# Kernel tuning notes

Hardware: AMD Instinct MI355X
Metric: run time of the kernel (lower is better)

## Reference

```python
import jax, jax.numpy as jnp
import numpy as np

EPS = 1e-6

def _ln(x):
    # LayerNorm without affine, biased variance (matches torch default)
    m = jnp.mean(x, axis=-1, keepdims=True)
    v = jnp.var(x, axis=-1, keepdims=True)
    return (x - m) / jnp.sqrt(v + EPS)

def setup_inputs() -> dict:
    key = jax.random.key(0)
    ks = jax.random.split(key, 12)
    B, N, C = 8, 4096, 768
    H = C * 4
    s = 0.02
    return {
        "x":   jax.random.normal(ks[0], (B, N, C), dtype=jnp.float32),
        "Wq":  jax.random.normal(ks[1], (C, C), dtype=jnp.float32) * s,
        "bq":  jnp.zeros((C,), dtype=jnp.float32),
        "Wkv": jax.random.normal(ks[2], (C, 2 * C), dtype=jnp.float32) * s,
        "bkv": jnp.zeros((2 * C,), dtype=jnp.float32),
        "Wo":  jax.random.normal(ks[3], (C, C), dtype=jnp.float32) * s,
        "bo":  jnp.zeros((C,), dtype=jnp.float32),
        "W1":  jax.random.normal(ks[4], (C, H), dtype=jnp.float32) * s,
        "b1":  jnp.zeros((H,), dtype=jnp.float32),
        "W2":  jax.random.normal(ks[5], (H, C), dtype=jnp.float32) * s,
        "b2":  jnp.zeros((C,), dtype=jnp.float32),
    }

def reference(x, Wq, bq, Wkv, bkv, Wo, bo, W1, b1, W2, b2):
    B, N, C = x.shape
    h = 16
    d = C // h
    scale = d ** -0.5

    xn = _ln(x)                          # norm1 over full sequence
    past = xn[:, :-1, :]                 # [B, N-1, C]
    cur = xn[:, -1, :]                   # [B, C]

    q = (cur @ Wq + bq).reshape(B, h, 1, d)                 # [B,h,1,d]
    kv = past @ Wkv + bkv                                   # [B,N-1,2C]
    k, v = jnp.split(kv, 2, axis=-1)
    k = k.reshape(B, N - 1, h, d).transpose(0, 2, 1, 3)     # [B,h,N-1,d]
    v = v.reshape(B, N - 1, h, d).transpose(0, 2, 1, 3)

    sim = jnp.einsum('bhqd,bhkd->bhqk', q, k) * scale       # [B,h,1,N-1]
    attn = jax.nn.softmax(sim, axis=-1)
    out = jnp.einsum('bhqk,bhkd->bhqd', attn, v)            # [B,h,1,d]
    out = out.transpose(0, 2, 1, 3).reshape(B, C)           # [B,C]
    out = out @ Wo + bo

    last = x[:, -1, :] + out                                # attn residual
    mlp = jax.nn.gelu(_ln(last) @ W1 + b1, approximate=True) @ W2 + b2
    last = last + mlp                                       # mlp residual

    return x.at[:, -1, :].set(last)
```

## Files before the change

kernel.cpp:

```cpp
#include <hip/hip_runtime.h>

#define B_ 8
#define N_ 4096
#define C_ 768
#define NP_ 4095
#define H_ 16
#define D_ 48
#define HID_ 3072
#define SCALE 0.14433756729740643f

typedef unsigned short u16;
typedef unsigned int u32;
typedef __attribute__((ext_vector_type(4))) float f32x4;
typedef __attribute__((ext_vector_type(8))) short short8;

__device__ __forceinline__ u32 f2bf_bits(float f){
  union { float f; u32 i; } v; v.f = f;
  return (v.i + 0x7fffu + ((v.i >> 16) & 1u)) >> 16;
}
__device__ __forceinline__ u16 f2bf(float f){ return (u16)f2bf_bits(f); }
__device__ __forceinline__ u32 pack2(float a, float b){
  return f2bf_bits(a) | (f2bf_bits(b) << 16);
}

__global__ __launch_bounds__(256) void k_q(const float* __restrict__ x,
    const float* __restrict__ Wq, const float* __restrict__ bq,
    float* __restrict__ qv)
{
  int b = blockIdx.y, t = threadIdx.x;
  int j0 = blockIdx.x*32;
  __shared__ float xs[C_];
  __shared__ float red[32][9];
  __shared__ float redA[4], redB[4];
  const float* xr = x + ((size_t)b*N_ + NP_)*C_;
  float v0 = xr[t], v1 = xr[t+256], v2 = xr[t+512];
  float s = v0+v1+v2, q = v0*v0+v1*v1+v2*v2;
  #pragma unroll
  for (int off=32; off; off>>=1){ s += __shfl_xor(s,off); q += __shfl_xor(q,off); }
  int w = t>>6, l = t&63;
  if (l==0){ redA[w]=s; redB[w]=q; }
  __syncthreads();
  s = redA[0]+redA[1]+redA[2]+redA[3];
  q = redB[0]+redB[1]+redB[2]+redB[3];
  float mean = s*(1.f/C_), var = q*(1.f/C_) - mean*mean;
  float rstd = rsqrtf(var + 1e-6f);
  xs[t] = (v0-mean)*rstd; xs[t+256] = (v1-mean)*rstd; xs[t+512] = (v2-mean)*rstd;
  __syncthreads();
  int jl = t&31, part = t>>5;
  const float* wp = Wq + (size_t)(part*96)*C_ + j0 + jl;
  const float* xp = xs + part*96;
  float acc = 0.f;
  #pragma unroll 8
  for (int c=0;c<96;c++) acc += xp[c]*wp[(size_t)c*C_];
  red[jl][part] = acc;
  __syncthreads();
  if (part==0){
    float a = bq[j0+jl];
    #pragma unroll
    for (int p=0;p<8;p++) a += red[jl][p];
    qv[(size_t)b*C_ + j0 + jl] = a;
  }
}

__global__ __launch_bounds__(256) void k_qw(const float* __restrict__ qv,
    const float* __restrict__ Wkv, u16* __restrict__ qWb)
{
  int b = blockIdx.y, t = threadIdx.x;
  int c0 = blockIdx.x*16;
  __shared__ float qs[C_];
  for (int u=t; u<C_; u+=256) qs[u] = qv[(size_t)b*C_+u];
  __syncthreads();
  int h = t&15, cl = t>>4;
  int c = c0 + cl;
  const float* wp = Wkv + (size_t)c*(2*C_) + h*D_;
  const float* qh = qs + h*D_;
  float acc = 0.f;
  #pragma unroll
  for (int d=0; d<D_; d++) acc += qh[d]*wp[d];
  qWb[((size_t)b*H_ + h)*C_ + c] = f2bf(acc);
}

__global__ __launch_bounds__(256) void k_pre(const float* __restrict__ x,
    const u16* __restrict__ qWb, float* __restrict__ outp,
    u16* __restrict__ wrsT, float* __restrict__ denom, float* __restrict__ corr)
{
  int b = blockIdx.y;
  int tid = threadIdx.x;
  int w = tid>>6, l = tid&63;
  int kblk = blockIdx.x*16;
  __shared__ u16 xn[16][776];
  __shared__ float2 stl[16];
  __shared__ float part[4][16][17];
  const size_t xb = (size_t)b*N_*C_;

  #pragma unroll
  for (int i=0;i<4;i++){
    int r = w*4 + i;
    int kt = kblk + r;
    const float4* rp = (const float4*)(x + xb + (size_t)kt*C_);
    float4* op = (float4*)(outp + xb + (size_t)kt*C_);
    float4 v0 = rp[l], v1 = rp[l+64], v2 = rp[l+128];
    op[l] = v0; op[l+64] = v1; op[l+128] = v2;
    float s = v0.x+v0.y+v0.z+v0.w + v1.x+v1.y+v1.z+v1.w + v2.x+v2.y+v2.z+v2.w;
    float q = v0.x*v0.x+v0.y*v0.y+v0.z*v0.z+v0.w*v0.w
            + v1.x*v1.x+v1.y*v1.y+v1.z*v1.z+v1.w*v1.w
            + v2.x*v2.x+v2.y*v2.y+v2.z*v2.z+v2.w*v2.w;
    #pragma unroll
    for (int off=32; off; off>>=1){ s += __shfl_xor(s,off); q += __shfl_xor(q,off); }
    float mean = s*(1.f/C_), var = q*(1.f/C_) - mean*mean;
    float rstd = rsqrtf(var + 1e-6f);
    if (l==0) stl[r] = make_float2(mean, rstd);
    u32* xrow = (u32*)&xn[r][0];
    xrow[2*l]       = pack2((v0.x-mean)*rstd, (v0.y-mean)*rstd);
    xrow[2*l+1]     = pack2((v0.z-mean)*rstd, (v0.w-mean)*rstd);
    xrow[128+2*l]   = pack2((v1.x-mean)*rstd, (v1.y-mean)*rstd);
    xrow[128+2*l+1] = pack2((v1.z-mean)*rstd, (v1.w-mean)*rstd);
    xrow[256+2*l]   = pack2((v2.x-mean)*rstd, (v2.y-mean)*rstd);
    xrow[256+2*l+1] = pack2((v2.z-mean)*rstd, (v2.w-mean)*rstd);
  }
  __syncthreads();

  {
    int arow = l&15;
    int ko = w*192 + (l>>4)*8;
    const u16* brb = qWb + ((size_t)b*H_ + (l&15))*C_ + ko;
    f32x4 acc = {0.f,0.f,0.f,0.f};
    #pragma unroll
    for (int s2=0;s2<6;s2++){
      union{uint4 u; short8 v;} A, Bf;
      A.u  = *(const uint4*)&xn[arow][ko + s2*32];
      Bf.u = *(const uint4*)(brb + s2*32);
      acc = __builtin_amdgcn_mfma_f32_16x16x32_bf16(A.v, Bf.v, acc, 0,0,0);
    }
    int mb = (l>>4)*4, n = l&15;
    #pragma unroll
    for (int r=0;r<4;r++) part[w][mb+r][n] = acc[r];
  }
  __syncthreads();

  {
    int m = tid>>4, n = tid&15;
    float sim = part[0][m][n] + part[1][m][n] + part[2][m][n] + part[3][m][n];
    int kt = kblk + m;
    float2 ms = stl[m];
    float wv = (kt < NP_) ? __expf(sim*SCALE) : 0.f;
    float wrs = wv * ms.y;
    wrsT[((size_t)b*H_ + n)*N_ + kt] = f2bf(wrs);
    part[0][m][n] = wv;
    part[1][m][n] = wrs * ms.x;
  }
  __syncthreads();
  if (tid < 16){
    float ds = 0.f, cs = 0.f;
    #pragma unroll
    for (int m=0;m<16;m++){ ds += part[0][m][tid]; cs += part[1][m][tid]; }
    atomicAdd(denom + (size_t)b*H_ + tid, ds);
    atomicAdd(corr  + (size_t)b*H_ + tid, cs);
  }
}

__global__ __launch_bounds__(256) void k_ctx2(const float* __restrict__ x,
    const u16* __restrict__ wrsT, float* __restrict__ ctx)
{
  int b = blockIdx.y;
  int cg = blockIdx.x % 12;
  int ks = blockIdx.x / 12;
  int tid = threadIdx.x;
  int w = tid>>6, l = tid&63;
  int ctile = cg*64 + w*16;
  int k0 = ks*512;
  const size_t xb = (size_t)b*N_*C_;
  const u16* ap = wrsT + ((size_t)b*H_ + (l&15))*N_ + k0 + (l>>4)*8;
  const float* bp = x + xb + (size_t)(k0 + (l>>4)*8)*C_ + ctile + (l&15);
  f32x4 acc = {0.f,0.f,0.f,0.f};
  for (int s=0;s<16;s++){
    union{uint4 u; short8 v;} A, Bf;
    A.u = *(const uint4*)(ap + s*32);
    const float* bq2 = bp + (size_t)s*32*C_;
    float x0 = bq2[0];
    float x1 = bq2[(size_t)1*C_];
    float x2 = bq2[(size_t)2*C_];
    float x3 = bq2[(size_t)3*C_];
    float x4 = bq2[(size_t)4*C_];
    float x5 = bq2[(size_t)5*C_];
    float x6 = bq2[(size_t)6*C_];
    float x7 = bq2[(size_t)7*C_];
    uint4 nb;
    nb.x = pack2(x0,x1); nb.y = pack2(x2,x3);
    nb.z = pack2(x4,x5); nb.w = pack2(x6,x7);
    Bf.u = nb;
    acc = __builtin_amdgcn_mfma_f32_16x16x32_bf16(A.v, Bf.v, acc, 0,0,0);
  }
  int cc = ctile + (l&15);
  float* cb = ctx + (size_t)b*H_*C_;
  #pragma unroll
  for (int r=0;r<4;r++){
    int h = (l>>4)*4 + r;
    atomicAdd(cb + h*C_ + cc, acc[r]);
  }
}

__global__ __launch_bounds__(256) void k_v(const float* __restrict__ ctx,
    const float* __restrict__ denom, const float* __restrict__ corr,
    const float* __restrict__ Wkv, const float* __restrict__ bkv,
    float* __restrict__ oat)
{
  int b = blockIdx.y, t = threadIdx.x;
  int t0 = blockIdx.x*32;
  int h0 = t0/D_;
  int h1 = (t0+31)/D_; if (h1 > H_-1) h1 = H_-1;
  __shared__ float cn[2][C_];
  __shared__ float red[32][9];
  float inv0 = 1.f/denom[(size_t)b*H_+h0];
  float inv1 = 1.f/denom[(size_t)b*H_+h1];
  float cr0 = corr[(size_t)b*H_+h0];
  float cr1 = corr[(size_t)b*H_+h1];
  for (int u=t; u<C_; u+=256){
    cn[0][u] = (ctx[((size_t)b*H_+h0)*C_+u] - cr0)*inv0;
    cn[1][u] = (ctx[((size_t)b*H_+h1)*C_+u] - cr1)*inv1;
  }
  __syncthreads();
  int jl = t&31, part = t>>5;
  int tt = t0 + jl;
  int hi = (tt/D_) - h0;
  const float* wp = Wkv + (size_t)(part*96)*(2*C_) + C_ + tt;
  const float* cp = cn[hi] + part*96;
  float acc = 0.f;
  #pragma unroll 8
  for (int c=0;c<96;c++) acc += cp[c]*wp[(size_t)c*(2*C_)];
  red[jl][part] = acc;
  __syncthreads();
  if (part==0){
    float a = bkv[C_ + tt];
    #pragma unroll
    for (int p=0;p<8;p++) a += red[jl][p];
    oat[(size_t)b*C_ + tt] = a;
  }
}

__global__ __launch_bounds__(256) void k_o(const float* __restrict__ x,
    const float* __restrict__ oat, const float* __restrict__ Wo,
    const float* __restrict__ bo, float* __restrict__ lastb)
{
  int b = blockIdx.y, t = threadIdx.x;
  int t0 = blockIdx.x*32;
  __shared__ float xs[C_];
  __shared__ float red[32][9];
  for (int u=t; u<C_; u+=256) xs[u] = oat[(size_t)b*C_+u];
  __syncthreads();
  int jl = t&31, part = t>>5;
  int tt = t0 + jl;
  const float* wp = Wo + (size_t)(part*96)*C_ + tt;
  const float* xp = xs + part*96;
  float acc = 0.f;
  #pragma unroll 8
  for (int c=0;c<96;c++) acc += xp[c]*wp[(size_t)c*C_];
  red[jl][part] = acc;
  __syncthreads();
  if (part==0){
    float a = bo[tt];
    #pragma unroll
    for (int p=0;p<8;p++) a += red[jl][p];
    lastb[(size_t)b*C_ + tt] = x[((size_t)b*N_ + NP_)*C_ + tt] + a;
  }
}

__global__ __launch_bounds__(256) void k_mlp1(const float* __restrict__ lastb,
    const float* __restrict__ W1, const float* __restrict__ b1,
    float* __restrict__ hid)
{
  int t = threadIdx.x;
  int j0 = blockIdx.x*16;
  __shared__ float xs[B_][C_];
  __shared__ float red[16][16][8];
  {
    int bb = t>>5, sub = t&31;
    const float* xr = lastb + (size_t)bb*C_;
    float s=0.f, q=0.f;
    #pragma unroll
    for (int j=0;j<24;j++){ float v = xr[sub+32*j]; s += v; q += v*v; }
    #pragma unroll
    for (int off=1; off<32; off<<=1){ s += __shfl_xor(s,off); q += __shfl_xor(q,off); }
    float mean = s*(1.f/C_), var = q*(1.f/C_) - mean*mean;
    float rstd = rsqrtf(var + 1e-6f);
    #pragma unroll
    for (int j=0;j<24;j++){ xs[bb][sub+32*j] = (xr[sub+32*j]-mean)*rstd; }
  }
  __syncthreads();
  int jl = t&15, part = t>>4;
  const float* wp = W1 + (size_t)(part*48)*HID_ + j0 + jl;
  float acc[B_];
  #pragma unroll
  for (int bb=0;bb<B_;bb++) acc[bb]=0.f;
  for (int c=0;c<48;c++){
    float wv = wp[(size_t)c*HID_];
    int cc = part*48 + c;
    #pragma unroll
    for (int bb=0;bb<B_;bb++) acc[bb] += xs[bb][cc]*wv;
  }
  #pragma unroll
  for (int bb=0;bb<B_;bb++) red[jl][part][bb] = acc[bb];
  __syncthreads();
  if (t < 128){
    int jl2 = t&15, bb = t>>4;
    float a = b1[j0+jl2];
    #pragma unroll
    for (int p=0;p<16;p++) a += red[jl2][p][bb];
    float t3 = a + 0.044715f*a*a*a;
    float g = 0.5f*a*(1.f + tanhf(0.7978845608f*t3));
    hid[(size_t)bb*HID_ + j0 + jl2] = g;
  }
}

__global__ __launch_bounds__(256) void k_mlp2(const float* __restrict__ hid,
    const float* __restrict__ W2, const float* __restrict__ b2,
    const float* __restrict__ lastb, float* __restrict__ outp)
{
  int t = threadIdx.x;
  int c0 = blockIdx.x*8;
  __shared__ float red[8][32][8];
  int ccl = t&7, part = t>>3;
  const float* wp = W2 + (size_t)(part*96)*C_ + c0 + ccl;
  float acc[B_];
  #pragma unroll
  for (int bb=0;bb<B_;bb++) acc[bb]=0.f;
  for (int j=0;j<96;j++){
    float wv = wp[(size_t)j*C_];
    int jj = part*96 + j;
    #pragma unroll
    for (int bb=0;bb<B_;bb++) acc[bb] += hid[(size_t)bb*HID_ + jj]*wv;
  }
  #pragma unroll
  for (int bb=0;bb<B_;bb++) red[ccl][part][bb] = acc[bb];
  __syncthreads();
  if (t < 64){
    int cc2 = t&7, bb = t>>3;
    float a = 0.f;
    #pragma unroll
    for (int p=0;p<32;p++) a += red[cc2][p][bb];
    int cc = c0 + cc2;
    a += b2[cc] + lastb[(size_t)bb*C_ + cc];
    outp[((size_t)bb*N_ + NP_)*C_ + cc] = a;
  }
}

extern "C" void kernel_launch(void* const* d_in, const int* in_sizes, int n_in,
                              void* d_out, int out_size, void* d_ws, size_t ws_size,
                              hipStream_t stream)
{
  (void)in_sizes; (void)n_in; (void)out_size; (void)ws_size;
  const float* x   = (const float*)d_in[0];
  const float* Wq  = (const float*)d_in[1];
  const float* bq  = (const float*)d_in[2];
  const float* Wkv = (const float*)d_in[3];
  const float* bkv = (const float*)d_in[4];
  const float* Wo  = (const float*)d_in[5];
  const float* bo  = (const float*)d_in[6];
  const float* W1  = (const float*)d_in[7];
  const float* b1  = (const float*)d_in[8];
  const float* W2  = (const float*)d_in[9];
  const float* b2  = (const float*)d_in[10];
  float* outp = (float*)d_out;
  float* ws = (float*)d_ws;
  float* ctx    = ws;
  float* denom  = ctx + 98304;
  float* corr   = denom + 128;
  float* qv     = corr + 128;
  float* oat    = qv + 6144;
  float* lastb  = oat + 6144;
  float* hid    = lastb + 6144;
  u16*   qWb    = (u16*)(hid + 24576);
  u16*   wrsT   = (u16*)(hid + 24576 + 49152);

  hipMemsetAsync(ctx, 0, (size_t)(98304+256)*sizeof(float), stream);
  hipLaunchKernelGGL(k_q,    dim3(24,B_), dim3(256), 0, stream, x, Wq, bq, qv);
  hipLaunchKernelGGL(k_qw,   dim3(48,B_), dim3(256), 0, stream, qv, Wkv, qWb);
  hipLaunchKernelGGL(k_pre,  dim3(256,B_), dim3(256), 0, stream, x, qWb, outp, wrsT, denom, corr);
  hipLaunchKernelGGL(k_ctx2, dim3(96,B_), dim3(256), 0, stream, x, wrsT, ctx);
  hipLaunchKernelGGL(k_v,    dim3(24,B_), dim3(256), 0, stream, ctx, denom, corr, Wkv, bkv, oat);
  hipLaunchKernelGGL(k_o,    dim3(24,B_), dim3(256), 0, stream, x, oat, Wo, bo, lastb);
  hipLaunchKernelGGL(k_mlp1, dim3(192), dim3(256), 0, stream, lastb, W1, b1, hid);
  hipLaunchKernelGGL(k_mlp2, dim3(96), dim3(256), 0, stream, hid, W2, b2, lastb, outp);
}
```

Baseline: 110.0 us.

## Fold workspace zeroing into k_q and load x directly into MFMA register layout in k_pre

```diff
diff --git a/kernel.cpp b/kernel.cpp
--- a/kernel.cpp
+++ b/kernel.cpp
@@ -19,16 +19,23 @@
   return (v.i + 0x7fffu + ((v.i >> 16) & 1u)) >> 16;
 }
 __device__ __forceinline__ u16 f2bf(float f){ return (u16)f2bf_bits(f); }
+__device__ __forceinline__ float bf2f(u16 u){
+  union { u32 i; float f; } v; v.i = ((u32)u) << 16; return v.f;
+}
 __device__ __forceinline__ u32 pack2(float a, float b){
   return f2bf_bits(a) | (f2bf_bits(b) << 16);
 }
 
 __global__ __launch_bounds__(256) void k_q(const float* __restrict__ x,
     const float* __restrict__ Wq, const float* __restrict__ bq,
-    float* __restrict__ qv)
+    float* __restrict__ qv, float* __restrict__ zbase)
 {
   int b = blockIdx.y, t = threadIdx.x;
   int j0 = blockIdx.x*32;
+  {
+    int gid = (b*24 + blockIdx.x)*256 + t;
+    for (int u = gid; u < 98560; u += 49152) zbase[u] = 0.f;
+  }
   __shared__ float xs[C_];
   __shared__ float red[32][9];
   __shared__ float redA[4], redB[4];
@@ -88,53 +95,57 @@
   int tid = threadIdx.x;
   int w = tid>>6, l = tid&63;
   int kblk = blockIdx.x*16;
-  __shared__ u16 xn[16][776];
+  __shared__ float smean[4][16], ssq[4][16];
   __shared__ float2 stl[16];
   __shared__ float part[4][16][17];
   const size_t xb = (size_t)b*N_*C_;
 
-  #pragma unroll
-  for (int i=0;i<4;i++){
-    int r = w*4 + i;
-    int kt = kblk + r;
-    const float4* rp = (const float4*)(x + xb + (size_t)kt*C_);
-    float4* op = (float4*)(outp + xb + (size_t)kt*C_);
-    float4 v0 = rp[l], v1 = rp[l+64], v2 = rp[l+128];
-    op[l] = v0; op[l+64] = v1; op[l+128] = v2;
-    float s = v0.x+v0.y+v0.z+v0.w + v1.x+v1.y+v1.z+v1.w + v2.x+v2.y+v2.z+v2.w;
-    float q = v0.x*v0.x+v0.y*v0.y+v0.z*v0.z+v0.w*v0.w
-            + v1.x*v1.x+v1.y*v1.y+v1.z*v1.z+v1.w*v1.w
-            + v2.x*v2.x+v2.y*v2.y+v2.z*v2.z+v2.w*v2.w;
-    #pragma unroll
-    for (int off=32; off; off>>=1){ s += __shfl_xor(s,off); q += __shfl_xor(q,off); }
-    float mean = s*(1.f/C_), var = q*(1.f/C_) - mean*mean;
-    float rstd = rsqrtf(var + 1e-6f);
-    if (l==0) stl[r] = make_float2(mean, rstd);
-    u32* xrow = (u32*)&xn[r][0];
-    xrow[2*l]       = pack2((v0.x-mean)*rstd, (v0.y-mean)*rstd);
-    xrow[2*l+1]     = pack2((v0.z-mean)*rstd, (v0.w-mean)*rstd);
-    xrow[128+2*l]   = pack2((v1.x-mean)*rstd, (v1.y-mean)*rstd);
-    xrow[128+2*l+1] = pack2((v1.z-mean)*rstd, (v1.w-mean)*rstd);
-    xrow[256+2*l]   = pack2((v2.x-mean)*rstd, (v2.y-mean)*rstd);
-    xrow[256+2*l+1] = pack2((v2.z-mean)*rstd, (v2.w-mean)*rstd);
-  }
-  __syncthreads();
-
+  int r = l & 15;
+  int row = kblk + r;
+  int cb = w*192 + ((l>>4)<<3);
+  const float* xp = x + xb + (size_t)row*C_ + cb;
+  float* op = outp + xb + (size_t)row*C_ + cb;
+
+  float4 g[12];
+  float s = 0.f, q = 0.f;
+  #pragma unroll
+  for (int s2=0; s2<6; ++s2){
+    float4 a0 = *(const float4*)(xp + s2*32);
+    float4 a1 = *(const float4*)(xp + s2*32 + 4);
+    g[2*s2] = a0; g[2*s2+1] = a1;
+    *(float4*)(op + s2*32)     = a0;
+    *(float4*)(op + s2*32 + 4) = a1;
+    s += a0.x+a0.y+a0.z+a0.w + a1.x+a1.y+a1.z+a1.w;
+    q += a0.x*a0.x+a0.y*a0.y+a0.z*a0.z+a0.w*a0.w
+       + a1.x*a1.x+a1.y*a1.y+a1.z*a1.z+a1.w*a1.w;
+  }
+  s += __shfl_xor(s,16); q += __shfl_xor(q,16);
+  s += __shfl_xor(s,32); q += __shfl_xor(q,32);
+  if (l < 16){ smean[w][l] = s; ssq[w][l] = q; }
+  __syncthreads();
+  float fs = smean[0][r]+smean[1][r]+smean[2][r]+smean[3][r];
+  float fq = ssq[0][r]+ssq[1][r]+ssq[2][r]+ssq[3][r];
+  float mean = fs*(1.f/C_), var = fq*(1.f/C_) - mean*mean;
+  float rstd = rsqrtf(var + 1e-6f);
+  if (tid < 16) stl[tid] = make_float2(mean, rstd);
+
+  const u16* brb = qWb + ((size_t)b*H_ + r)*C_ + cb;
+  f32x4 acc = {0.f,0.f,0.f,0.f};
+  #pragma unroll
+  for (int s2=0;s2<6;s2++){
+    float4 a0 = g[2*s2], a1 = g[2*s2+1];
+    union{uint4 u; short8 v;} A, Bf;
+    A.u.x = pack2((a0.x-mean)*rstd, (a0.y-mean)*rstd);
+    A.u.y = pack2((a0.z-mean)*rstd, (a0.w-mean)*rstd);
+    A.u.z = pack2((a1.x-mean)*rstd, (a1.y-mean)*rstd);
+    A.u.w = pack2((a1.z-mean)*rstd, (a1.w-mean)*rstd);
+    Bf.u = *(const uint4*)(brb + s2*32);
+    acc = __builtin_amdgcn_mfma_f32_16x16x32_bf16(A.v, Bf.v, acc, 0,0,0);
+  }
   {
-    int arow = l&15;
-    int ko = w*192 + (l>>4)*8;
-    const u16* brb = qWb + ((size_t)b*H_ + (l&15))*C_ + ko;
-    f32x4 acc = {0.f,0.f,0.f,0.f};
-    #pragma unroll
-    for (int s2=0;s2<6;s2++){
-      union{uint4 u; short8 v;} A, Bf;
-      A.u  = *(const uint4*)&xn[arow][ko + s2*32];
-      Bf.u = *(const uint4*)(brb + s2*32);
-      acc = __builtin_amdgcn_mfma_f32_16x16x32_bf16(A.v, Bf.v, acc, 0,0,0);
-    }
     int mb = (l>>4)*4, n = l&15;
     #pragma unroll
-    for (int r=0;r<4;r++) part[w][mb+r][n] = acc[r];
+    for (int r4=0;r4<4;r4++) part[w][mb+r4][n] = acc[r4];
   }
   __syncthreads();
 
@@ -144,10 +155,10 @@
     int kt = kblk + m;
     float2 ms = stl[m];
     float wv = (kt < NP_) ? __expf(sim*SCALE) : 0.f;
-    float wrs = wv * ms.y;
-    wrsT[((size_t)b*H_ + n)*N_ + kt] = f2bf(wrs);
+    u16 wb = f2bf(wv * ms.y);
+    wrsT[((size_t)b*H_ + n)*N_ + kt] = wb;
     part[0][m][n] = wv;
-    part[1][m][n] = wrs * ms.x;
+    part[1][m][n] = bf2f(wb) * ms.x;
   }
   __syncthreads();
   if (tid < 16){
@@ -372,8 +383,7 @@
   u16*   qWb    = (u16*)(hid + 24576);
   u16*   wrsT   = (u16*)(hid + 24576 + 49152);
 
-  hipMemsetAsync(ctx, 0, (size_t)(98304+256)*sizeof(float), stream);
-  hipLaunchKernelGGL(k_q,    dim3(24,B_), dim3(256), 0, stream, x, Wq, bq, qv);
+  hipLaunchKernelGGL(k_q,    dim3(24,B_), dim3(256), 0, stream, x, Wq, bq, qv, ctx);
   hipLaunchKernelGGL(k_qw,   dim3(48,B_), dim3(256), 0, stream, qv, Wkv, qWb);
   hipLaunchKernelGGL(k_pre,  dim3(256,B_), dim3(256), 0, stream, x, qWb, outp, wrsT, denom, corr);
   hipLaunchKernelGGL(k_ctx2, dim3(96,B_), dim3(256), 0, stream, x, wrsT, ctx);
```

Result: no change. 109.7 us (-0.3%).
